# Optimization experiments

Measured on AMD Instinct MI355X. Metric: run time of the kernel, lower is better.

## Reference

```python
import jax, jax.numpy as jnp
import numpy as np

B, S, HID = 2, 2048, 1024
H, KV, D = 16, 8, 64
NDIM = 2          # position_ids.shape[-1]
EPS = 1e-6
SCALING = 1.0


def _rms_norm(x, w=None, eps=EPS):
    # matches _RMSNorm: fp32 compute, optional learnable scale
    xf = x.astype(jnp.float32)
    n = xf * jax.lax.rsqrt(jnp.mean(xf * xf, axis=-1, keepdims=True) + eps)
    if w is not None:
        n = n * w.astype(jnp.float32)
    return n.astype(x.dtype)


def _rotate_half(x):
    d = x.shape[-1] // 2
    return jnp.concatenate([-x[..., d:], x[..., :d]], axis=-1)


def _apply_multidim_rope(x, cos, sin, ndim):
    # x: [B,S,h,D]; cos/sin: [B,S,D]; unsqueeze_dim=2 broadcasts over heads
    num_channels = x.shape[-1]
    cpd = 2 * (num_channels // (2 * ndim))  # channels per RoPE dimension
    outs = []
    for k in range(ndim):
        sl = slice(k * cpd, (k + 1) * cpd)
        xk = x[..., sl]
        ck = cos[..., sl][:, :, None, :]
        sk = sin[..., sl][:, :, None, :]
        outs.append(xk * ck + _rotate_half(xk) * sk)
    return jnp.concatenate(outs, axis=-1)


def setup_inputs() -> dict:
    key = jax.random.key(0)
    ks = jax.random.split(key, 10)
    scale = 0.02
    return {
        "hidden_states": jax.random.normal(ks[0], (B, S, HID), jnp.float32),
        "cos": jax.random.normal(ks[1], (B, S, D), jnp.float32),
        "sin": jax.random.normal(ks[2], (B, S, D), jnp.float32),
        "position_ids": jax.random.randint(ks[3], (B, S, NDIM), 0, 64, jnp.int64),
        "Wq": jax.random.normal(ks[4], (HID, H * D), jnp.float32) * scale,
        "Wk": jax.random.normal(ks[5], (HID, KV * D), jnp.float32) * scale,
        "Wv": jax.random.normal(ks[6], (HID, KV * D), jnp.float32) * scale,
        "Wo": jax.random.normal(ks[7], (H * D, HID), jnp.float32) * scale,
        "q_norm_w": jnp.ones((D,), jnp.float32),
        "k_norm_w": jnp.ones((D,), jnp.float32),
    }


def reference(hidden_states, cos, sin, position_ids, Wq, Wk, Wv, Wo, q_norm_w, k_norm_w):
    ndim = position_ids.shape[-1]
    bsz, seq_len, _ = hidden_states.shape

    q = (hidden_states @ Wq).reshape(bsz, seq_len, H, D)
    q = _rms_norm(q, q_norm_w)
    q = _apply_multidim_rope(q, cos, sin, ndim)
    q = jnp.transpose(q, (0, 2, 1, 3))  # [B,H,S,D]

    k = (hidden_states @ Wk).reshape(bsz, seq_len, KV, D)
    k = _rms_norm(k, k_norm_w)
    k = _apply_multidim_rope(k, cos, sin, ndim)
    k = jnp.transpose(k, (0, 2, 1, 3))  # [B,KV,S,D]

    v = (hidden_states @ Wv).reshape(bsz, seq_len, KV, D)
    v = _rms_norm(v, None)  # v_norm has no scale
    v = jnp.transpose(v, (0, 2, 1, 3))  # [B,KV,S,D]

    groups = H // KV
    if groups > 1:
        k = jnp.repeat(k, groups, axis=1)  # [B,H,S,D]
        v = jnp.repeat(v, groups, axis=1)

    scores = jnp.einsum("bhqd,bhkd->bhqk", q, k) * SCALING
    attn = jax.nn.softmax(scores.astype(jnp.float32), axis=-1).astype(q.dtype)
    out = jnp.einsum("bhqk,bhkd->bhqd", attn, v)
    out = jnp.transpose(out, (0, 2, 1, 3)).reshape(bsz, seq_len, H * D)
    return out @ Wo
```

## Files before the change

### kernel.cpp

```cpp
#include <hip/hip_runtime.h>

#define PB 2
#define PS 2048
#define PHID 1024
#define PH 16
#define PKV 8
#define PD 64
#define PM (PB*PS)
#define PR (PB*PH*PS)

typedef _Float16 f16_t;
typedef _Float16 f16x8 __attribute__((ext_vector_type(8)));
typedef _Float16 f16x2 __attribute__((ext_vector_type(2)));
typedef float f32x4 __attribute__((ext_vector_type(4)));

#define MFMAH(a,b,c)  __builtin_amdgcn_mfma_f32_16x16x32_f16((a),(b),(c),0,0,0)
#define LOG2E 1.44269504f

__device__ __forceinline__ void gl16(const f16_t* g, f16_t* l) {
  __builtin_amdgcn_global_load_lds(
      (const __attribute__((address_space(1))) void*)g,
      (__attribute__((address_space(3))) void*)l, 16, 0, 0);
}

__global__ __launch_bounds__(256)
void convert_hs(const float* __restrict__ hs, f16_t* __restrict__ hf)
{
  const size_t i = ((size_t)blockIdx.x * 256 + threadIdx.x) * 8;
  float4 a = *(const float4*)&hs[i];
  float4 b = *(const float4*)&hs[i + 4];
  float xs[8] = {a.x, a.y, a.z, a.w, b.x, b.y, b.z, b.w};
  f16x8 v;
  #pragma unroll
  for (int j = 0; j < 8; ++j) v[j] = (f16_t)xs[j];
  *(f16x8*)&hf[i] = v;
}

__global__ __launch_bounds__(256)
void convert_w(const float* __restrict__ Wq, const float* __restrict__ Wk,
               const float* __restrict__ Wv, const float* __restrict__ Wo,
               f16_t* __restrict__ wtT)
{
  __shared__ float Tt[64][68];
  const int tid = threadIdx.x;
  const int slot = blockIdx.x >> 4, k0 = (blockIdx.x & 15) * 64;

  const float* src; int N, ncol0, orow0;
  if (slot < 16)      { src = Wq; N = 1024; ncol0 = slot*64;      orow0 = slot*64; }
  else if (slot < 24) { src = Wk; N = 512;  ncol0 = (slot-16)*64; orow0 = 1024 + (slot-16)*64; }
  else if (slot < 32) { src = Wv; N = 512;  ncol0 = (slot-24)*64; orow0 = 1536 + (slot-24)*64; }
  else                { src = Wo; N = 1024; ncol0 = (slot-32)*64; orow0 = 2048 + (slot-32)*64; }

  const int tk = tid >> 6, tn = tid & 63;
  #pragma unroll
  for (int i = 0; i < 16; ++i)
    Tt[tn][tk*16 + i] = src[(size_t)(k0 + tk*16 + i) * N + ncol0 + tn];
  __syncthreads();

  const int n = tid >> 2, kc = (tid & 3) * 16;
  f16x8 a0, a1;
  #pragma unroll
  for (int i = 0; i < 8; ++i) {
    a0[i] = (f16_t)Tt[n][kc + i];
    a1[i] = (f16_t)Tt[n][kc + 8 + i];
  }
  const size_t ob = (size_t)(orow0 + n) * 1024 + k0 + kc;
  *(f16x8*)&wtT[ob]     = a0;
  *(f16x8*)&wtT[ob + 8] = a1;
}

__global__ __launch_bounds__(256)
void qkv_kernel(const f16_t* __restrict__ hsf, const f16_t* __restrict__ wtT,
                const float* __restrict__ cosp, const float* __restrict__ sinp,
                const float* __restrict__ qnw, const float* __restrict__ knw,
                f16_t* __restrict__ q_o, f16_t* __restrict__ k_o,
                f16_t* __restrict__ vt_o)
{
  __shared__ __align__(16) f16_t Ah[128][64];
  __shared__ __align__(16) f16_t Bh[64][64];

  const int tid = threadIdx.x;
  const int lane = tid & 63, wave = tid >> 6;
  const int lo16 = lane & 15, hi4 = lane >> 4;
  const int lin = blockIdx.x;
  const int swz = (lin & 7) * 128 + (lin >> 3);
  const int m0 = (swz >> 5) * 128;
  const int slot = swz & 31;

  int kind, hd, orow;
  if (slot < 16)      { kind = 0; hd = slot;      orow = slot*64; }
  else if (slot < 24) { kind = 1; hd = slot - 16; orow = 1024 + hd*64; }
  else                { kind = 2; hd = slot - 24; orow = 1536 + hd*64; }

  f32x4 acc[2][4];
  #pragma unroll
  for (int qb = 0; qb < 2; ++qb)
    #pragma unroll
    for (int j = 0; j < 4; ++j) acc[qb][j] = f32x4{0.f, 0.f, 0.f, 0.f};

  const int ri = lane >> 3, pc = lane & 7;
  const int lcs = (pc ^ ri) * 8;
  size_t aoff[2]; f16_t* aldst[2];
  #pragma unroll
  for (int q = 0; q < 2; ++q) {
    aoff[q] = (size_t)(m0 + wave*32 + q*16 + (ri & 7) + (q*0)) * PHID + lcs;
    aldst[q] = &Ah[wave*32 + q*16][0];
  }
  size_t aoff4[4]; f16_t* aldst4[4];
  #pragma unroll
  for (int q = 0; q < 4; ++q) {
    aoff4[q] = (size_t)(m0 + wave*32 + q*8 + ri) * PHID + lcs;
    aldst4[q] = &Ah[wave*32 + q*8][0];
  }
  size_t boff[2]; int brow[2];
  #pragma unroll
  for (int q = 0; q < 2; ++q) {
    brow[q] = wave*16 + q*8;
    boff[q] = (size_t)(orow + brow[q] + ri) * 1024 + lcs;
  }

  const int rsw = lo16 & 7;

  for (int k0 = 0; k0 < PHID; k0 += 64) {
    __syncthreads();
    #pragma unroll
    for (int q = 0; q < 4; ++q) gl16(hsf + aoff4[q] + k0, aldst4[q]);
    #pragma unroll
    for (int q = 0; q < 2; ++q) gl16(wtT + boff[q] + k0, &Bh[brow[q]][0]);
    __syncthreads();

    #pragma unroll
    for (int t = 0; t < 2; ++t) {
      const int ccol = ((t*4 + hi4) ^ rsw) * 8;
      f16x8 ah[2];
      #pragma unroll
      for (int qb = 0; qb < 2; ++qb)
        ah[qb] = *(const f16x8*)&Ah[wave*32 + qb*16 + lo16][ccol];
      #pragma unroll
      for (int j = 0; j < 4; ++j) {
        f16x8 bh = *(const f16x8*)&Bh[j*16 + lo16][ccol];
        #pragma unroll
        for (int qb = 0; qb < 2; ++qb)
          acc[qb][j] = MFMAH(ah[qb], bh, acc[qb][j]);
      }
    }
  }

  #pragma unroll
  for (int qb = 0; qb < 2; ++qb) {
    float scale[4];
    #pragma unroll
    for (int r = 0; r < 4; ++r) {
      float s = 0.f;
      #pragma unroll
      for (int j = 0; j < 4; ++j) s += acc[qb][j][r] * acc[qb][j][r];
      #pragma unroll
      for (int m = 1; m < 16; m <<= 1) s += __shfl_xor(s, m);
      scale[r] = 1.0f / sqrtf(s * (1.0f/64.0f) + 1e-6f);
    }
    float nw[4];
    #pragma unroll
    for (int j = 0; j < 4; ++j)
      nw[j] = (kind == 0) ? qnw[lo16 + 16*j] : (kind == 1 ? knw[lo16 + 16*j] : 1.0f);

    float y[4][4];
    #pragma unroll
    for (int j = 0; j < 4; ++j)
      #pragma unroll
      for (int r = 0; r < 4; ++r) y[j][r] = acc[qb][j][r] * scale[r] * nw[j];

    if (kind == 2) {
      #pragma unroll
      for (int r = 0; r < 4; ++r) {
        int mg = m0 + wave*32 + qb*16 + hi4*4 + r;
        int b = mg >> 11, sq = mg & 2047;
        #pragma unroll
        for (int j = 0; j < 4; ++j) {
          int d = lo16 + 16*j;
          vt_o[((size_t)((b*PKV + hd)*PD + d))*PS + sq] = (f16_t)y[j][r];
        }
      }
    } else {
      #pragma unroll
      for (int r = 0; r < 4; ++r) {
        int mg = m0 + wave*32 + qb*16 + hi4*4 + r;
        int b = mg >> 11, sq = mg & 2047;
        const float* cp = &cosp[(size_t)mg * PD];
        const float* sp = &sinp[(size_t)mg * PD];
        float z[4];
        #pragma unroll
        for (int j = 0; j < 4; ++j) {
          float c = cp[lo16 + 16*j], s = sp[lo16 + 16*j];
          float rot = (j & 1) ? y[j-1][r] : -y[j+1][r];
          z[j] = y[j][r] * c + rot * s;
        }
        #pragma unroll
        for (int j = 0; j < 4; ++j) {
          int d = lo16 + 16*j;
          if (kind == 0) {
            size_t idx = ((size_t)(b*PH + hd)*PS + sq)*PD + d;
            q_o[idx] = (f16_t)(z[j] * LOG2E);
          } else {
            size_t idx = ((size_t)(b*PKV + hd)*PS + sq)*PD + d;
            k_o[idx] = (f16_t)z[j];
          }
        }
      }
    }
  }
}

__global__ __launch_bounds__(256, 4)
void attn_kernel(const f16_t* __restrict__ q_g, const f16_t* __restrict__ k_g,
                 const f16_t* __restrict__ vt_g,
                 f16_t* __restrict__ op, float2* __restrict__ ml)
{
  __shared__ __align__(16) f16_t Ks[64][72];
  __shared__ __align__(16) f16_t Vs[64][72];
  __shared__ __align__(16) f16_t Ps[128][72];

  const int tid = threadIdx.x, lane = tid & 63, wave = tid >> 6;
  const int lo16 = lane & 15, hi4 = lane >> 4;
  const int lin = blockIdx.x;
  const int swz = (lin & 7) * 128 + (lin >> 3);
  const int qt = swz & 15;
  const int bh = (swz >> 4) & 31;
  const int ks = swz >> 9;
  const int b = bh >> 4, h = bh & 15, kvh = h >> 1;

  f16x8 qf[2][2];
  #pragma unroll
  for (int qb = 0; qb < 2; ++qb) {
    const size_t qbase = ((size_t)(b*PH + h)*PS + qt*128 + wave*32 + qb*16 + lo16) * PD;
    #pragma unroll
    for (int t = 0; t < 2; ++t)
      qf[qb][t] = *(const f16x8*)&q_g[qbase + t*32 + hi4*8];
  }

  f32x4 o[2][4];
  float mq[2] = {-1e30f, -1e30f}, lq[2] = {0.f, 0.f};
  #pragma unroll
  for (int qb = 0; qb < 2; ++qb)
    #pragma unroll
    for (int j = 0; j < 4; ++j) o[qb][j] = f32x4{0.f, 0.f, 0.f, 0.f};

  const int srow = tid >> 2, sc = (tid & 3) * 16;
  const size_t kbase = (size_t)(b*PKV + kvh) * PS * PD + (size_t)ks * 1024 * PD;
  const size_t vbase = (size_t)(b*PKV + kvh) * PD * PS + (size_t)ks * 1024;

  f16x8 gk0, gk1, gv0, gv1;
  auto LOADT = [&](int kt) {
    const f16_t* kp = &k_g[kbase + (size_t)(kt*64 + srow)*PD + sc];
    const f16_t* vp = &vt_g[vbase + (size_t)srow*PS + kt*64 + sc];
    gk0 = *(const f16x8*)kp;  gk1 = *(const f16x8*)(kp + 8);
    gv0 = *(const f16x8*)vp;  gv1 = *(const f16x8*)(vp + 8);
  };
  LOADT(0);

  for (int kt = 0; kt < 16; ++kt) {
    __syncthreads();
    *(f16x8*)&Ks[srow][sc]     = gk0;
    *(f16x8*)&Ks[srow][sc + 8] = gk1;
    *(f16x8*)&Vs[srow][sc]     = gv0;
    *(f16x8*)&Vs[srow][sc + 8] = gv1;
    if (kt + 1 < 16) LOADT(kt + 1);
    __syncthreads();

    f32x4 sacc[2][4];
    #pragma unroll
    for (int qb = 0; qb < 2; ++qb)
      #pragma unroll
      for (int j = 0; j < 4; ++j) sacc[qb][j] = f32x4{0.f, 0.f, 0.f, 0.f};
    __builtin_amdgcn_s_setprio(1);
    #pragma unroll
    for (int j = 0; j < 4; ++j) {
      #pragma unroll
      for (int t = 0; t < 2; ++t) {
        f16x8 kf = *(const f16x8*)&Ks[j*16 + lo16][t*32 + hi4*8];
        #pragma unroll
        for (int qb = 0; qb < 2; ++qb)
          sacc[qb][j] = MFMAH(kf, qf[qb][t], sacc[qb][j]);
      }
    }
    __builtin_amdgcn_s_setprio(0);

    #pragma unroll
    for (int qb = 0; qb < 2; ++qb) {
      float tm = sacc[qb][0][0];
      #pragma unroll
      for (int j = 0; j < 4; ++j)
        #pragma unroll
        for (int r = 0; r < 4; ++r) tm = fmaxf(tm, sacc[qb][j][r]);
      tm = fmaxf(tm, __shfl_xor(tm, 16));
      tm = fmaxf(tm, __shfl_xor(tm, 32));
      if (!__all(tm <= mq[qb] + 8.0f)) {
        float mnew = fmaxf(mq[qb], tm);
        float alpha = __builtin_amdgcn_exp2f(mq[qb] - mnew);
        lq[qb] *= alpha;
        #pragma unroll
        for (int jd = 0; jd < 4; ++jd) o[qb][jd] *= alpha;
        mq[qb] = mnew;
      }
      float ls = 0.f;
      #pragma unroll
      for (int j = 0; j < 4; ++j)
        #pragma unroll
        for (int r = 0; r < 4; ++r) {
          float p = __builtin_amdgcn_exp2f(sacc[qb][j][r] - mq[qb]);
          sacc[qb][j][r] = p;
          ls += p;
        }
      ls += __shfl_xor(ls, 16);
      ls += __shfl_xor(ls, 32);
      lq[qb] += ls;
    }

    #pragma unroll
    for (int qb = 0; qb < 2; ++qb)
      #pragma unroll
      for (int j = 0; j < 4; ++j)
        #pragma unroll
        for (int rp = 0; rp < 2; ++rp)
          *(f16x2*)&Ps[wave*32 + qb*16 + lo16][j*16 + hi4*4 + 2*rp] =
              f16x2{(f16_t)sacc[qb][j][2*rp], (f16_t)sacc[qb][j][2*rp+1]};

    f16x8 pa[2][2];
    #pragma unroll
    for (int qb = 0; qb < 2; ++qb)
      #pragma unroll
      for (int t = 0; t < 2; ++t)
        pa[qb][t] = *(const f16x8*)&Ps[wave*32 + qb*16 + lo16][t*32 + hi4*8];

    __builtin_amdgcn_s_setprio(1);
    #pragma unroll
    for (int jd = 0; jd < 4; ++jd) {
      #pragma unroll
      for (int t = 0; t < 2; ++t) {
        f16x8 vf = *(const f16x8*)&Vs[jd*16 + lo16][t*32 + hi4*8];
        #pragma unroll
        for (int qb = 0; qb < 2; ++qb)
          o[qb][jd] = MFMAH(vf, pa[qb][t], o[qb][jd]);
      }
    }
    __builtin_amdgcn_s_setprio(0);
  }

  const int rbase = bh*PS + qt*128 + wave*32;
  if (hi4 == 0) {
    #pragma unroll
    for (int qb = 0; qb < 2; ++qb)
      ml[(size_t)ks*PR + rbase + qb*16 + lo16] = float2{mq[qb], lq[qb]};
  }
  #pragma unroll
  for (int qb = 0; qb < 2; ++qb) {
    float inv = 1.0f / lq[qb];
    #pragma unroll
    for (int jd = 0; jd < 4; ++jd)
      #pragma unroll
      for (int rp = 0; rp < 2; ++rp)
        *(f16x2*)&Ps[wave*32 + qb*16 + lo16][jd*16 + hi4*4 + 2*rp] =
            f16x2{(f16_t)(o[qb][jd][2*rp] * inv), (f16_t)(o[qb][jd][2*rp+1] * inv)};
  }
  {
    const int row = lane >> 1, half = lane & 1;
    const size_t gb_ = ((size_t)ks*PR + rbase + row) * PD + half*32;
    #pragma unroll
    for (int c = 0; c < 4; ++c)
      *(f16x8*)&op[gb_ + c*8] = *(const f16x8*)&Ps[wave*32 + row][half*32 + c*8];
  }
}

__global__ __launch_bounds__(256)
void merge_kernel(const f16_t* __restrict__ op, const float2* __restrict__ ml,
                  f16_t* __restrict__ ao)
{
  const int gid = blockIdx.x * 256 + threadIdx.x;
  const int row = gid >> 3, oct = gid & 7;
  float2 e0 = ml[row], e1 = ml[PR + row];
  float M = fmaxf(e0.x, e1.x);
  float c0 = __builtin_amdgcn_exp2f(e0.x - M) * e0.y;
  float c1 = __builtin_amdgcn_exp2f(e1.x - M) * e1.y;
  float inv = 1.0f / (c0 + c1);
  c0 *= inv; c1 *= inv;
  f16x8 a = *(const f16x8*)&op[(size_t)row*PD + oct*8];
  f16x8 bq = *(const f16x8*)&op[(size_t)(PR + row)*PD + oct*8];
  f16x8 r;
  #pragma unroll
  for (int i = 0; i < 8; ++i)
    r[i] = (f16_t)(c0 * (float)a[i] + c1 * (float)bq[i]);
  const int bh = row >> 11, sq = row & 2047;
  const int b = bh >> 4, h = bh & 15;
  *(f16x8*)&ao[((size_t)(b*PS + sq))*PHID + h*PD + oct*8] = r;
}

__global__ __launch_bounds__(256)
void oproj_kernel(const f16_t* __restrict__ ao, const f16_t* __restrict__ woT,
                  float* __restrict__ out)
{
  __shared__ __align__(16) f16_t As[128][40], Bs[64][40];
  const int tid = threadIdx.x;
  const int lane = tid & 63, wave = tid >> 6;
  const int lo16 = lane & 15, hi4 = lane >> 4;
  const int lin = blockIdx.x;
  const int swz = (lin & 7) * 64 + (lin >> 3);
  const int m0 = (swz >> 4) * 128;
  const int col0 = (swz & 15) * 64;

  f32x4 acc[2][4];
  #pragma unroll
  for (int qb = 0; qb < 2; ++qb)
    #pragma unroll
    for (int j = 0; j < 4; ++j) acc[qb][j] = f32x4{0.f, 0.f, 0.f, 0.f};

  const int ar = tid >> 1, akc = (tid & 1) * 16;
  const int bn = tid & 63, bkc = (tid >> 6) * 8;

  f16x8 gA0, gA1, gB;
  auto LOADA = [&](int k0) {
    const f16_t* ap = &ao[(size_t)(m0 + ar) * PHID + k0 + akc];
    gA0 = *(const f16x8*)ap;
    gA1 = *(const f16x8*)(ap + 8);
  };
  auto LOADB = [&](int k0) {
    gB = *(const f16x8*)&woT[(size_t)(col0 + bn) * 1024 + k0 + bkc];
  };
  LOADA(0); LOADB(0);

  for (int k0 = 0; k0 < PHID; k0 += 32) {
    __syncthreads();
    *(f16x8*)&As[ar][akc]     = gA0;
    *(f16x8*)&As[ar][akc + 8] = gA1;
    *(f16x8*)&Bs[bn][bkc]     = gB;
    if (k0 + 32 < PHID) { LOADA(k0 + 32); LOADB(k0 + 32); }
    __syncthreads();
    {
      f16x8 a[2];
      #pragma unroll
      for (int qb = 0; qb < 2; ++qb)
        a[qb] = *(const f16x8*)&As[wave*32 + qb*16 + lo16][hi4*8];
      #pragma unroll
      for (int j = 0; j < 4; ++j) {
        f16x8 bb = *(const f16x8*)&Bs[j*16 + lo16][hi4*8];
        #pragma unroll
        for (int qb = 0; qb < 2; ++qb)
          acc[qb][j] = MFMAH(a[qb], bb, acc[qb][j]);
      }
    }
  }

  #pragma unroll
  for (int qb = 0; qb < 2; ++qb)
    #pragma unroll
    for (int r = 0; r < 4; ++r) {
      int mg = m0 + wave*32 + qb*16 + hi4*4 + r;
      #pragma unroll
      for (int j = 0; j < 4; ++j)
        out[(size_t)mg*PHID + col0 + lo16 + 16*j] = acc[qb][j][r];
    }
}

extern "C" void kernel_launch(void* const* d_in, const int* in_sizes, int n_in,
                              void* d_out, int out_size, void* d_ws, size_t ws_size,
                              hipStream_t stream) {
  (void)in_sizes; (void)n_in; (void)out_size; (void)ws_size;
  const float* hs   = (const float*)d_in[0];
  const float* cosp = (const float*)d_in[1];
  const float* sinp = (const float*)d_in[2];
  const float* Wq   = (const float*)d_in[4];
  const float* Wk   = (const float*)d_in[5];
  const float* Wv   = (const float*)d_in[6];
  const float* Wo   = (const float*)d_in[7];
  const float* qnw  = (const float*)d_in[8];
  const float* knw  = (const float*)d_in[9];
  float* out = (float*)d_out;

  const size_t QN = (size_t)PB*PH*PS*PD;
  const size_t KN = (size_t)PB*PKV*PS*PD;
  const size_t HN = (size_t)PM*PHID;
  char* wsb = (char*)d_ws;
  f16_t*  qv  = (f16_t*)wsb;
  f16_t*  kv  = qv + QN;
  f16_t*  vt  = kv + KN;
  f16_t*  hsf = vt + KN;
  f16_t*  wtT = hsf + HN;
  f16_t*  op  = wtT + (size_t)3072*1024;
  float2* ml  = (float2*)(op + 2*QN);
  f16_t*  ao  = qv;
  const f16_t* woT = wtT + (size_t)2048*1024;

  convert_hs<<<dim3(2048), 256, 0, stream>>>(hs, hsf);
  convert_w <<<dim3(768),  256, 0, stream>>>(Wq, Wk, Wv, Wo, wtT);
  qkv_kernel<<<dim3(1024), 256, 0, stream>>>(hsf, wtT, cosp, sinp,
                                             qnw, knw, qv, kv, vt);
  attn_kernel<<<dim3(1024), 256, 0, stream>>>(qv, kv, vt, op, ml);
  merge_kernel<<<dim3(PR*8/256), 256, 0, stream>>>(op, ml, ao);
  oproj_kernel<<<dim3(512), 256, 0, stream>>>(ao, woT, out);
}
```

Before: 131.2 us.

## Double-buffer K/V via direct global-to-LDS loads and keep P in registers

New measurement: 126.6 us. -3.5%, faster.

```diff
diff --git a/kernel.cpp b/kernel.cpp
--- a/kernel.cpp
+++ b/kernel.cpp
@@ -100,12 +100,6 @@
 
   const int ri = lane >> 3, pc = lane & 7;
   const int lcs = (pc ^ ri) * 8;
-  size_t aoff[2]; f16_t* aldst[2];
-  #pragma unroll
-  for (int q = 0; q < 2; ++q) {
-    aoff[q] = (size_t)(m0 + wave*32 + q*16 + (ri & 7) + (q*0)) * PHID + lcs;
-    aldst[q] = &Ah[wave*32 + q*16][0];
-  }
   size_t aoff4[4]; f16_t* aldst4[4];
   #pragma unroll
   for (int q = 0; q < 4; ++q) {
@@ -174,10 +168,14 @@
       for (int r = 0; r < 4; ++r) {
         int mg = m0 + wave*32 + qb*16 + hi4*4 + r;
         int b = mg >> 11, sq = mg & 2047;
+        int g = sq & 63;
+        int sp = (g & 3) | (((g >> 4) & 1) << 2) | (((g >> 2) & 1) << 3)
+               | (((g >> 3) & 1) << 4) | (g & 32);
+        int sq2 = (sq & ~63) | sp;
         #pragma unroll
         for (int j = 0; j < 4; ++j) {
           int d = lo16 + 16*j;
-          vt_o[((size_t)((b*PKV + hd)*PD + d))*PS + sq] = (f16_t)y[j][r];
+          vt_o[((size_t)((b*PKV + hd)*PD + d))*PS + sq2] = (f16_t)y[j][r];
         }
       }
     } else {
@@ -215,9 +213,10 @@
                  const f16_t* __restrict__ vt_g,
                  f16_t* __restrict__ op, float2* __restrict__ ml)
 {
-  __shared__ __align__(16) f16_t Ks[64][72];
-  __shared__ __align__(16) f16_t Vs[64][72];
-  __shared__ __align__(16) f16_t Ps[128][72];
+  __shared__ __align__(16) char lds_raw[32768];
+  f16_t (*Ks)[64][64] = (f16_t (*)[64][64])lds_raw;
+  f16_t (*Vs)[64][64] = (f16_t (*)[64][64])(lds_raw + 16384);
+  f16_t (*Ob)[72]     = (f16_t (*)[72])lds_raw;
 
   const int tid = threadIdx.x, lane = tid & 63, wave = tid >> 6;
   const int lo16 = lane & 15, hi4 = lane >> 4;
@@ -244,27 +243,29 @@
     #pragma unroll
     for (int j = 0; j < 4; ++j) o[qb][j] = f32x4{0.f, 0.f, 0.f, 0.f};
 
-  const int srow = tid >> 2, sc = (tid & 3) * 16;
+  const int ri = lane >> 3;
+  const int lcs = ((lane & 7) ^ ri) * 8;
   const size_t kbase = (size_t)(b*PKV + kvh) * PS * PD + (size_t)ks * 1024 * PD;
   const size_t vbase = (size_t)(b*PKV + kvh) * PD * PS + (size_t)ks * 1024;
 
-  f16x8 gk0, gk1, gv0, gv1;
-  auto LOADT = [&](int kt) {
-    const f16_t* kp = &k_g[kbase + (size_t)(kt*64 + srow)*PD + sc];
-    const f16_t* vp = &vt_g[vbase + (size_t)srow*PS + kt*64 + sc];
-    gk0 = *(const f16x8*)kp;  gk1 = *(const f16x8*)(kp + 8);
-    gv0 = *(const f16x8*)vp;  gv1 = *(const f16x8*)(vp + 8);
+  auto STAGE = [&](int kt, int buf) {
+    const f16_t* kp = k_g + kbase + (size_t)kt * 64 * PD;
+    const f16_t* vp = vt_g + vbase + kt * 64;
+    #pragma unroll
+    for (int i = 0; i < 2; ++i) {
+      const int st = wave*2 + i;
+      gl16(kp + (st*8 + ri)*PD + lcs, &Ks[buf][st*8][0]);
+      gl16(vp + (size_t)(st*8 + ri)*PS + lcs, &Vs[buf][st*8][0]);
+    }
   };
-  LOADT(0);
+
+  STAGE(0, 0);
+  int cur = 0;
+  const int rsw = lo16 & 7;
 
   for (int kt = 0; kt < 16; ++kt) {
     __syncthreads();
-    *(f16x8*)&Ks[srow][sc]     = gk0;
-    *(f16x8*)&Ks[srow][sc + 8] = gk1;
-    *(f16x8*)&Vs[srow][sc]     = gv0;
-    *(f16x8*)&Vs[srow][sc + 8] = gv1;
-    if (kt + 1 < 16) LOADT(kt + 1);
-    __syncthreads();
+    if (kt + 1 < 16) STAGE(kt + 1, cur ^ 1);
 
     f32x4 sacc[2][4];
     #pragma unroll
@@ -276,7 +277,7 @@
     for (int j = 0; j < 4; ++j) {
       #pragma unroll
       for (int t = 0; t < 2; ++t) {
-        f16x8 kf = *(const f16x8*)&Ks[j*16 + lo16][t*32 + hi4*8];
+        f16x8 kf = *(const f16x8*)&Ks[cur][j*16 + lo16][((t*4 + hi4) ^ rsw) * 8];
         #pragma unroll
         for (int qb = 0; qb < 2; ++qb)
           sacc[qb][j] = MFMAH(kf, qf[qb][t], sacc[qb][j]);
@@ -315,36 +316,35 @@
       lq[qb] += ls;
     }
 
+    f16x8 pa[2][2];
     #pragma unroll
     for (int qb = 0; qb < 2; ++qb)
       #pragma unroll
-      for (int j = 0; j < 4; ++j)
-        #pragma unroll
-        for (int rp = 0; rp < 2; ++rp)
-          *(f16x2*)&Ps[wave*32 + qb*16 + lo16][j*16 + hi4*4 + 2*rp] =
-              f16x2{(f16_t)sacc[qb][j][2*rp], (f16_t)sacc[qb][j][2*rp+1]};
-
-    f16x8 pa[2][2];
-    #pragma unroll
-    for (int qb = 0; qb < 2; ++qb)
-      #pragma unroll
-      for (int t = 0; t < 2; ++t)
-        pa[qb][t] = *(const f16x8*)&Ps[wave*32 + qb*16 + lo16][t*32 + hi4*8];
+      for (int t = 0; t < 2; ++t) {
+        f16x8 v;
+        #pragma unroll
+        for (int e = 0; e < 8; ++e)
+          v[e] = (f16_t)sacc[qb][2*t + (e >> 2)][e & 3];
+        pa[qb][t] = v;
+      }
 
     __builtin_amdgcn_s_setprio(1);
     #pragma unroll
     for (int jd = 0; jd < 4; ++jd) {
       #pragma unroll
       for (int t = 0; t < 2; ++t) {
-        f16x8 vf = *(const f16x8*)&Vs[jd*16 + lo16][t*32 + hi4*8];
+        f16x8 vf = *(const f16x8*)&Vs[cur][jd*16 + lo16][((t*4 + hi4) ^ rsw) * 8];
         #pragma unroll
         for (int qb = 0; qb < 2; ++qb)
           o[qb][jd] = MFMAH(vf, pa[qb][t], o[qb][jd]);
       }
     }
     __builtin_amdgcn_s_setprio(0);
-  }
-
+
+    cur ^= 1;
+  }
+
+  __syncthreads();
   const int rbase = bh*PS + qt*128 + wave*32;
   if (hi4 == 0) {
     #pragma unroll
@@ -358,7 +358,7 @@
     for (int jd = 0; jd < 4; ++jd)
       #pragma unroll
       for (int rp = 0; rp < 2; ++rp)
-        *(f16x2*)&Ps[wave*32 + qb*16 + lo16][jd*16 + hi4*4 + 2*rp] =
+        *(f16x2*)&Ob[wave*32 + qb*16 + lo16][jd*16 + hi4*4 + 2*rp] =
             f16x2{(f16_t)(o[qb][jd][2*rp] * inv), (f16_t)(o[qb][jd][2*rp+1] * inv)};
   }
   {
@@ -366,7 +366,7 @@
     const size_t gb_ = ((size_t)ks*PR + rbase + row) * PD + half*32;
     #pragma unroll
     for (int c = 0; c < 4; ++c)
-      *(f16x8*)&op[gb_ + c*8] = *(const f16x8*)&Ps[wave*32 + row][half*32 + c*8];
+      *(f16x8*)&op[gb_ + c*8] = *(const f16x8*)&Ob[wave*32 + row][half*32 + c*8];
   }
 }
 
```
